# Optimization experiments

Measured on AMD Instinct MI355X. Metric: run time of the kernel, lower is better.

The kernel has to match this reference:

```python
import math
import jax, jax.numpy as jnp
import numpy as np

B, H, L, E = 2, 8, 2048, 64
MEM, LMEM = 512, 0
KV = L + MEM + LMEM


def rel_shift(x):
    # x: [..., i, j] -> Transformer-XL relative shift, output [..., i, j]
    *lead, i, j = x.shape
    x = jnp.concatenate([x, jnp.zeros((*lead, i, i), x.dtype)], axis=-1)  # [..., i, i+j]
    l = i + j - 1
    flat = x.reshape(*lead, i * (i + j))
    pad = (-flat.shape[-1]) % l
    flat = jnp.concatenate([flat, jnp.zeros((*lead, pad), x.dtype)], axis=-1)
    shifted = flat.reshape(*lead, -1, l)
    return shifted[..., :i, i - 1:]


def setup_inputs() -> dict:
    key = jax.random.key(0)
    kq, kk, kv, kp = jax.random.split(key, 4)
    return {
        "q": jax.random.normal(kq, (B, H, L, E), jnp.float32),
        "k": jax.random.normal(kk, (B, H, KV, E), jnp.float32),
        "v": jax.random.normal(kv, (B, H, KV, E), jnp.float32),
        "attn_mask": 0,
        "pos_emb": jax.random.normal(kp, (H, KV, E), jnp.float32),
        "kv_len": KV,
        "mem_len": MEM,
        "lmem_len": LMEM,
    }


def reference(q, k, v, attn_mask, pos_emb, kv_len, mem_len, lmem_len):
    b, h, l, e = q.shape
    scale = 1.0 / math.sqrt(e)
    dots = jnp.einsum('bhid,bhjd->bhij', q, k) * scale  # [B,H,L,KV]
    # relative-position bias
    pe = pos_emb[:, -kv_len:].astype(q.dtype)  # [H,KV,E]
    pos_dots = jnp.einsum('bhid,hjd->bhij', q, pe) * scale
    pos_dots = rel_shift(pos_dots)
    pad = dots.shape[-1] - pos_dots.shape[-1]
    pos_dots = jnp.pad(pos_dots, ((0, 0), (0, 0), (0, 0), (pad, 0)))
    dots = dots + pos_dots
    # memory-aware causal mask: [L, L+total_mem], triu at diag 1+total_mem
    total_mem = mem_len + lmem_len
    mask = jnp.triu(jnp.ones((l, l + total_mem), bool), k=1 + total_mem)
    neg = -jnp.finfo(dots.dtype).max
    dots = jnp.where(mask[None, None], neg, dots)
    attn = jax.nn.softmax(dots, axis=-1)  # dropout is identity at eval
    out = jnp.einsum('bhij,bhjd->bhid', attn, v)
    return out.transpose(0, 2, 1, 3).reshape(b, l, h * e)
```

## Files before the change

### kernel.cpp

```cpp
#include <hip/hip_runtime.h>
#include <hip/hip_bf16.h>

typedef __bf16 bf16;
typedef __attribute__((ext_vector_type(8))) __bf16 bf16x8;
typedef __attribute__((ext_vector_type(4))) __bf16 bf16x4;
typedef __attribute__((ext_vector_type(2))) __bf16 bf16x2;
typedef __attribute__((ext_vector_type(4))) float f32x4;

#define NB 2
#define NH 8
#define NL 2048
#define NE 64
#define NKV 2560

#define QN (NB*NH*NL*NE)
#define KN (NB*NH*NKV*NE)
#define VN KN
#define PEN (NH*NKV*NE)

#define MFMA(a,b,c) __builtin_amdgcn_mfma_f32_16x16x32_bf16(a,b,c,0,0,0)

template<int CTRL>
__device__ __forceinline__ float fdpp(float x) {
  return __builtin_bit_cast(float,
    __builtin_amdgcn_update_dpp(0, __builtin_bit_cast(int, x), CTRL, 0xF, 0xF, true));
}
__device__ __forceinline__ float rowmax16(float x) {
  x = fmaxf(x, fdpp<0x121>(x));
  x = fmaxf(x, fdpp<0x122>(x));
  x = fmaxf(x, fdpp<0x124>(x));
  x = fmaxf(x, fdpp<0x128>(x));
  return x;
}
__device__ __forceinline__ float rowsum16(float x) {
  x += fdpp<0x121>(x);
  x += fdpp<0x122>(x);
  x += fdpp<0x124>(x);
  x += fdpp<0x128>(x);
  return x;
}

extern "C" __global__ __launch_bounds__(256) void cvt_kernel(
    const float* __restrict__ q, const float* __restrict__ k,
    const float* __restrict__ v, const float* __restrict__ pe,
    bf16* __restrict__ ws)
{
  long i = ((long)blockIdx.x * 256 + threadIdx.x) * 8;
  const float* __restrict__ src;
  long off;
  if (i < QN)            { src = q;  off = i; }
  else if (i < QN+KN)    { src = k;  off = i - QN; }
  else if (i < QN+KN+VN) { src = v;  off = i - (QN+KN); }
  else                   { src = pe; off = i - (QN+KN+VN); }
  float4 f0 = *(const float4*)(src + off);
  float4 f1 = *(const float4*)(src + off + 4);
  bf16x8 o = { (bf16)f0.x, (bf16)f0.y, (bf16)f0.z, (bf16)f0.w,
               (bf16)f1.x, (bf16)f1.y, (bf16)f1.z, (bf16)f1.w };
  *(bf16x8*)(ws + i) = o;
}

extern "C" __global__ __launch_bounds__(256, 2) void attn_kernel(
    const bf16* __restrict__ qb, const bf16* __restrict__ kb,
    const bf16* __restrict__ vb, const bf16* __restrict__ peb,
    float* __restrict__ out)
{
  __shared__ bf16 Klds[64][72];
  __shared__ bf16 Vtlds[64][72];
  __shared__ bf16 PElds[128][72];
  __shared__ bf16 Plds[4][16][72];

  const int tid  = threadIdx.x;
  const int wave = tid >> 6;
  const int lane = tid & 63;
  const int g    = lane >> 4;
  const int c    = lane & 15;

  const int id   = blockIdx.x;
  const int jm   = id & 255;
  const int half = id >> 8;
  const int qtile = half ? (jm & 31) : (31 - (jm & 31));
  const int hb = (half << 3) | (jm >> 5);
  const int h  = hb & 7;
  const int b  = hb >> 3;
  const int bh = b * NH + h;
  const int r0  = qtile * 64;
  const int r0w = r0 + wave * 16;

  const bf16* __restrict__ qB  = qb  + (size_t)bh * NL  * NE;
  const bf16* __restrict__ kB  = kb  + (size_t)bh * NKV * NE;
  const bf16* __restrict__ vB  = vb  + (size_t)bh * NKV * NE;
  const bf16* __restrict__ peB = peb + (size_t)h  * NKV * NE;

  bf16x8 aq[2];
#pragma unroll
  for (int ks = 0; ks < 2; ++ks)
    aq[ks] = *(const bf16x8*)(qB + (size_t)(r0w + c) * NE + ks*32 + g*8);

  const f32x4 ZERO = {0.f, 0.f, 0.f, 0.f};
  f32x4 O[4];
  float M2[4], Lsum[4];
#pragma unroll
  for (int i = 0; i < 4; ++i) { O[i] = ZERO; M2[i] = -3.0e38f; Lsum[i] = 0.f; }

  const int ntiles = qtile + 9;
  const float COMB = 0.125f * 1.44269504088896f;

  bf16x8 sk0, sk1, svv0, svv1, spe0, spe1, spe2, spe3;
  const int krow = tid >> 2, kseg = tid & 3;
  const int vp   = tid >> 3, vcg  = tid & 7;
  const int perow = tid >> 1, peseg = tid & 1;

#define LOADT(m0_, pebase_) do {                                             \
    { const bf16* s = kB + (size_t)((m0_) + krow) * NE + kseg * 16;          \
      sk0 = *(const bf16x8*)(s); sk1 = *(const bf16x8*)(s + 8); }            \
    { const bf16* s = vB + (size_t)((m0_) + 2*vp) * NE + vcg * 8;            \
      svv0 = *(const bf16x8*)(s); svv1 = *(const bf16x8*)(s + NE); }         \
    { int prw = (pebase_) + perow;                                           \
      prw = prw < (NKV-1) ? prw : (NKV-1);                                   \
      const bf16* s = peB + (size_t)prw * NE + peseg * 32;                   \
      spe0 = *(const bf16x8*)(s);      spe1 = *(const bf16x8*)(s + 8);       \
      spe2 = *(const bf16x8*)(s + 16); spe3 = *(const bf16x8*)(s + 24); }    \
  } while (0)

  const int pebase0 = 1984 - r0;
  LOADT(0, pebase0);

  for (int t = 0; t < ntiles; ++t) {
    const int m0 = t * 64;

    __syncthreads();
    *(bf16x8*)&Klds[krow][kseg*16]   = sk0;
    *(bf16x8*)&Klds[krow][kseg*16+8] = sk1;
    {
      const int colw = (2*vp) ^ (vcg << 3);
#pragma unroll
      for (int i2 = 0; i2 < 8; ++i2) {
        bf16x2 pr = { svv0[i2], svv1[i2] };
        *(bf16x2*)&Vtlds[vcg*8 + i2][colw] = pr;
      }
    }
    *(bf16x8*)&PElds[perow][peseg*32]      = spe0;
    *(bf16x8*)&PElds[perow][peseg*32 + 8]  = spe1;
    *(bf16x8*)&PElds[perow][peseg*32 + 16] = spe2;
    *(bf16x8*)&PElds[perow][peseg*32 + 24] = spe3;
    __syncthreads();

    if (t + 1 < ntiles) LOADT(m0 + 64, pebase0 + m0 + 64);

    f32x4 S[4];
#pragma unroll
    for (int sub = 0; sub < 4; ++sub) {
      S[sub] = ZERO;
#pragma unroll
      for (int ks = 0; ks < 2; ++ks) {
        bf16x8 bk = *(const bf16x8*)&Klds[sub*16 + c][ks*32 + g*8];
        S[sub] = MFMA(aq[ks], bk, S[sub]);
      }
    }
    f32x4 PP[5];
    {
      const int bo = 48 - wave * 16;
#pragma unroll
      for (int sub = 0; sub < 5; ++sub) {
        PP[sub] = ZERO;
#pragma unroll
        for (int ks = 0; ks < 2; ++ks) {
          bf16x8 bp = *(const bf16x8*)&PElds[bo + sub*16 + c][ks*32 + g*8];
          PP[sub] = MFMA(aq[ks], bp, PP[sub]);
        }
      }
    }

    float sv[4][4];
#pragma unroll
    for (int reg = 0; reg < 4; ++reg) {
      const int qr = g*4 + reg;
      const int srcc = (c - qr + 15) & 15;
      float sh[5];
#pragma unroll
      for (int s5 = 0; s5 < 5; ++s5) sh[s5] = __shfl(PP[s5][reg], srcc, 16);
      const bool sel = (c > qr);
#pragma unroll
      for (int sub = 0; sub < 4; ++sub) {
        const float bias = sel ? sh[sub+1] : sh[sub];
        sv[sub][reg] = (S[sub][reg] + bias) * COMB;
      }
    }
    if (t == ntiles - 1) {
#pragma unroll
      for (int sub = 0; sub < 4; ++sub)
#pragma unroll
        for (int reg = 0; reg < 4; ++reg)
          if (sub*16 + c > wave*16 + g*4 + reg) sv[sub][reg] = -3.0e38f;
    }

    float pexp[4][4];
#pragma unroll
    for (int reg = 0; reg < 4; ++reg) {
      float m2 = fmaxf(fmaxf(sv[0][reg], sv[1][reg]), fmaxf(sv[2][reg], sv[3][reg]));
      m2 = rowmax16(m2);
      const float Mn = fmaxf(M2[reg], m2);
      const float alpha = exp2f(M2[reg] - Mn);
      float rs = 0.f;
#pragma unroll
      for (int sub = 0; sub < 4; ++sub) {
        float p = exp2f(sv[sub][reg] - Mn);
        pexp[sub][reg] = p;
        rs += p;
      }
      rs = rowsum16(rs);
      Lsum[reg] = Lsum[reg] * alpha + rs;
      M2[reg] = Mn;
#pragma unroll
      for (int es = 0; es < 4; ++es) O[es][reg] *= alpha;
    }

#pragma unroll
    for (int sub = 0; sub < 4; ++sub)
#pragma unroll
      for (int reg = 0; reg < 4; ++reg)
        Plds[wave][g*4 + reg][sub*16 + c] = (bf16)pexp[sub][reg];

    __builtin_amdgcn_wave_barrier();

#pragma unroll
    for (int ks = 0; ks < 2; ++ks) {
      bf16x8 ap = *(const bf16x8*)&Plds[wave][c][ks*32 + g*8];
#pragma unroll
      for (int es = 0; es < 4; ++es) {
        const int vrow = es*16 + c;
        const int vcol = (ks*32 + g*8) ^ ((vrow >> 3) << 3);
        bf16x8 bv = *(const bf16x8*)&Vtlds[vrow][vcol];
        O[es] = MFMA(ap, bv, O[es]);
      }
    }
  }

  float rinv[4];
#pragma unroll
  for (int reg = 0; reg < 4; ++reg) rinv[reg] = 1.0f / Lsum[reg];
#pragma unroll
  for (int es = 0; es < 4; ++es)
#pragma unroll
    for (int reg = 0; reg < 4; ++reg) {
      const int r = r0w + g*4 + reg;
      out[((size_t)b * NL + r) * (NH*NE) + h * NE + es*16 + c] = O[es][reg] * rinv[reg];
    }
}

extern "C" void kernel_launch(void* const* d_in, const int* in_sizes, int n_in,
                              void* d_out, int out_size, void* d_ws, size_t ws_size,
                              hipStream_t stream)
{
  const float* q  = (const float*)d_in[0];
  const float* k  = (const float*)d_in[1];
  const float* v  = (const float*)d_in[2];
  const float* pe = (const float*)d_in[4];
  float* out = (float*)d_out;
  bf16* ws = (bf16*)d_ws;

  cvt_kernel<<<4224, 256, 0, stream>>>(q, k, v, pe, ws);
  attn_kernel<<<512, 256, 0, stream>>>(
      ws, ws + QN, ws + QN + KN, ws + QN + KN + VN, out);
}
```

Before: 164.3 us.

## Pre-transpose V in convert kernel and double-buffer tiles via direct global-to-LDS loads

The convert kernel now writes V in a transposed [E][KV] layout through an LDS tile transpose, so the attention kernel no longer has to transpose V element-by-element into shared memory. The attention kernel stages K, V^T and positional-embedding tiles straight into double-buffered, XOR-swizzled LDS using global_load_lds, and overlaps the next tile's load with the current tile's compute using raw s_barrier and vmcnt waits. This removes the register round trip and the scattered bf16x2 LDS writes. In exchange it doubles LDS use, which may lower occupancy, and it relies on hand-written waitcnt counts being correct.

```diff
diff --git a/kernel.cpp b/kernel.cpp
--- a/kernel.cpp
+++ b/kernel.cpp
@@ -3,8 +3,6 @@
 
 typedef __bf16 bf16;
 typedef __attribute__((ext_vector_type(8))) __bf16 bf16x8;
-typedef __attribute__((ext_vector_type(4))) __bf16 bf16x4;
-typedef __attribute__((ext_vector_type(2))) __bf16 bf16x2;
 typedef __attribute__((ext_vector_type(4))) float f32x4;
 
 #define NB 2
@@ -19,6 +17,10 @@
 #define PEN (NH*NKV*NE)
 
 #define MFMA(a,b,c) __builtin_amdgcn_mfma_f32_16x16x32_bf16(a,b,c,0,0,0)
+
+#define GLOAD16(gp, lp) __builtin_amdgcn_global_load_lds(                   \
+    (const __attribute__((address_space(1))) void*)(gp),                    \
+    (__attribute__((address_space(3))) void*)(lp), 16, 0, 0)
 
 template<int CTRL>
 __device__ __forceinline__ float fdpp(float x) {
@@ -45,35 +47,68 @@
     const float* __restrict__ v, const float* __restrict__ pe,
     bf16* __restrict__ ws)
 {
-  long i = ((long)blockIdx.x * 256 + threadIdx.x) * 8;
-  const float* __restrict__ src;
-  long off;
-  if (i < QN)            { src = q;  off = i; }
-  else if (i < QN+KN)    { src = k;  off = i - QN; }
-  else if (i < QN+KN+VN) { src = v;  off = i - (QN+KN); }
-  else                   { src = pe; off = i - (QN+KN+VN); }
-  float4 f0 = *(const float4*)(src + off);
-  float4 f1 = *(const float4*)(src + off + 4);
-  bf16x8 o = { (bf16)f0.x, (bf16)f0.y, (bf16)f0.z, (bf16)f0.w,
-               (bf16)f1.x, (bf16)f1.y, (bf16)f1.z, (bf16)f1.w };
-  *(bf16x8*)(ws + i) = o;
+  __shared__ bf16 T[64][72];
+  const int bid = blockIdx.x, tid = threadIdx.x;
+  if (bid < 2944) {
+    long j = (long)bid * 2048 + tid * 8;
+    const float* __restrict__ src; bf16* __restrict__ dst;
+    if (j < QN)          { src = q + j;            dst = ws + j; }
+    else if (j < QN+KN)  { src = k + (j - QN);     dst = ws + j; }
+    else                 { src = pe + (j - QN - KN); dst = ws + j + VN; }
+    float4 f0 = *(const float4*)(src);
+    float4 f1 = *(const float4*)(src + 4);
+    bf16x8 o = { (bf16)f0.x, (bf16)f0.y, (bf16)f0.z, (bf16)f0.w,
+                 (bf16)f1.x, (bf16)f1.y, (bf16)f1.z, (bf16)f1.w };
+    *(bf16x8*)dst = o;
+  } else {
+    const int tb = bid - 2944;
+    const int bh = tb / 40, kt = tb % 40;
+    const float* __restrict__ vB = v + ((size_t)bh * NKV + kt * 64) * NE;
+    bf16* __restrict__ vT = ws + QN + KN + (size_t)bh * NE * NKV;
+    const int key = tid >> 2, e0 = (tid & 3) * 16;
+    const int sw = ((key >> 4) & 3) << 1;
+    const float* s = vB + (size_t)key * NE + e0;
+#pragma unroll
+    for (int j2 = 0; j2 < 2; ++j2) {
+      float4 fa = *(const float4*)(s + j2 * 8);
+      float4 fb = *(const float4*)(s + j2 * 8 + 4);
+      bf16x8 o = { (bf16)fa.x, (bf16)fa.y, (bf16)fa.z, (bf16)fa.w,
+                   (bf16)fb.x, (bf16)fb.y, (bf16)fb.z, (bf16)fb.w };
+      const int ch = (tid & 3) * 2 + j2;
+      *(bf16x8*)&T[key][(ch ^ sw) * 8] = o;
+    }
+    __syncthreads();
+    const int e = tid >> 2, ks0 = (tid & 3) * 16;
+#pragma unroll
+    for (int j2 = 0; j2 < 2; ++j2) {
+      bf16x8 o;
+#pragma unroll
+      for (int i = 0; i < 8; ++i) {
+        const int K = ks0 + j2 * 8 + i;
+        const int pos = (e >> 3) ^ (((K >> 4) & 3) << 1);
+        o[i] = T[K][pos * 8 + (e & 7)];
+      }
+      *(bf16x8*)&vT[(size_t)e * NKV + kt * 64 + ks0 + j2 * 8] = o;
+    }
+  }
 }
 
 extern "C" __global__ __launch_bounds__(256, 2) void attn_kernel(
     const bf16* __restrict__ qb, const bf16* __restrict__ kb,
-    const bf16* __restrict__ vb, const bf16* __restrict__ peb,
+    const bf16* __restrict__ vtb, const bf16* __restrict__ peb,
     float* __restrict__ out)
 {
-  __shared__ bf16 Klds[64][72];
-  __shared__ bf16 Vtlds[64][72];
-  __shared__ bf16 PElds[128][72];
-  __shared__ bf16 Plds[4][16][72];
+  __shared__ __align__(16) bf16 Kd[2][64][64];
+  __shared__ __align__(16) bf16 Vd[2][64][64];
+  __shared__ __align__(16) bf16 PEd[2][128][64];
+  __shared__ __align__(16) bf16 Plds[4][16][72];
 
   const int tid  = threadIdx.x;
   const int wave = tid >> 6;
   const int lane = tid & 63;
   const int g    = lane >> 4;
   const int c    = lane & 15;
+  const int cx   = c & 7;
 
   const int id   = blockIdx.x;
   const int jm   = id & 255;
@@ -88,7 +123,7 @@
 
   const bf16* __restrict__ qB  = qb  + (size_t)bh * NL  * NE;
   const bf16* __restrict__ kB  = kb  + (size_t)bh * NKV * NE;
-  const bf16* __restrict__ vB  = vb  + (size_t)bh * NKV * NE;
+  const bf16* __restrict__ vB  = vtb + (size_t)bh * NE  * NKV;
   const bf16* __restrict__ peB = peb + (size_t)h  * NKV * NE;
 
   bf16x8 aq[2];
@@ -104,48 +139,41 @@
 
   const int ntiles = qtile + 9;
   const float COMB = 0.125f * 1.44269504088896f;
-
-  bf16x8 sk0, sk1, svv0, svv1, spe0, spe1, spe2, spe3;
-  const int krow = tid >> 2, kseg = tid & 3;
-  const int vp   = tid >> 3, vcg  = tid & 7;
-  const int perow = tid >> 1, peseg = tid & 1;
-
-#define LOADT(m0_, pebase_) do {                                             \
-    { const bf16* s = kB + (size_t)((m0_) + krow) * NE + kseg * 16;          \
-      sk0 = *(const bf16x8*)(s); sk1 = *(const bf16x8*)(s + 8); }            \
-    { const bf16* s = vB + (size_t)((m0_) + 2*vp) * NE + vcg * 8;            \
-      svv0 = *(const bf16x8*)(s); svv1 = *(const bf16x8*)(s + NE); }         \
-    { int prw = (pebase_) + perow;                                           \
-      prw = prw < (NKV-1) ? prw : (NKV-1);                                   \
-      const bf16* s = peB + (size_t)prw * NE + peseg * 32;                   \
-      spe0 = *(const bf16x8*)(s);      spe1 = *(const bf16x8*)(s + 8);       \
-      spe2 = *(const bf16x8*)(s + 16); spe3 = *(const bf16x8*)(s + 24); }    \
+  const int pebase0 = 1984 - r0;
+
+  const int lr = lane >> 3;
+  const int lc = (lane & 7) ^ lr;
+
+#define STAGE(buf_, m0_, pebase_) do {                                         \
+    _Pragma("unroll")                                                          \
+    for (int j_ = 0; j_ < 2; ++j_) {                                           \
+      const int rb_ = (wave*2 + j_)*8;                                         \
+      GLOAD16(kB + (size_t)((m0_) + rb_ + lr)*NE + lc*8, &Kd[buf_][rb_][0]);   \
+      GLOAD16(vB + (size_t)(rb_ + lr)*NKV + (m0_) + lc*8, &Vd[buf_][rb_][0]);  \
+    }                                                                          \
+    _Pragma("unroll")                                                          \
+    for (int j_ = 0; j_ < 4; ++j_) {                                           \
+      const int rb_ = (wave*4 + j_)*8;                                         \
+      int prw_ = (pebase_) + rb_ + lr;                                         \
+      prw_ = prw_ < (NKV-1) ? prw_ : (NKV-1);                                  \
+      GLOAD16(peB + (size_t)prw_*NE + lc*8, &PEd[buf_][rb_][0]);               \
+    }                                                                          \
   } while (0)
 
-  const int pebase0 = 1984 - r0;
-  LOADT(0, pebase0);
+  STAGE(0, 0, pebase0);
 
   for (int t = 0; t < ntiles; ++t) {
-    const int m0 = t * 64;
-
-    __syncthreads();
-    *(bf16x8*)&Klds[krow][kseg*16]   = sk0;
-    *(bf16x8*)&Klds[krow][kseg*16+8] = sk1;
-    {
-      const int colw = (2*vp) ^ (vcg << 3);
-#pragma unroll
-      for (int i2 = 0; i2 < 8; ++i2) {
-        bf16x2 pr = { svv0[i2], svv1[i2] };
-        *(bf16x2*)&Vtlds[vcg*8 + i2][colw] = pr;
-      }
-    }
-    *(bf16x8*)&PElds[perow][peseg*32]      = spe0;
-    *(bf16x8*)&PElds[perow][peseg*32 + 8]  = spe1;
-    *(bf16x8*)&PElds[perow][peseg*32 + 16] = spe2;
-    *(bf16x8*)&PElds[perow][peseg*32 + 24] = spe3;
-    __syncthreads();
-
-    if (t + 1 < ntiles) LOADT(m0 + 64, pebase0 + m0 + 64);
+    const int cur = t & 1;
+    const int m0  = t * 64;
+
+    asm volatile("s_barrier" ::: "memory");
+    if (t + 1 < ntiles) {
+      STAGE(cur ^ 1, m0 + 64, pebase0 + m0 + 64);
+      asm volatile("s_waitcnt vmcnt(8)" ::: "memory");
+    } else {
+      asm volatile("s_waitcnt vmcnt(0)" ::: "memory");
+    }
+    asm volatile("s_barrier" ::: "memory");
 
     f32x4 S[4];
 #pragma unroll
@@ -153,7 +181,7 @@
       S[sub] = ZERO;
 #pragma unroll
       for (int ks = 0; ks < 2; ++ks) {
-        bf16x8 bk = *(const bf16x8*)&Klds[sub*16 + c][ks*32 + g*8];
+        bf16x8 bk = *(const bf16x8*)&Kd[cur][sub*16 + c][((ks*4 + g) ^ cx) * 8];
         S[sub] = MFMA(aq[ks], bk, S[sub]);
       }
     }
@@ -165,7 +193,7 @@
         PP[sub] = ZERO;
 #pragma unroll
         for (int ks = 0; ks < 2; ++ks) {
-          bf16x8 bp = *(const bf16x8*)&PElds[bo + sub*16 + c][ks*32 + g*8];
+          bf16x8 bp = *(const bf16x8*)&PEd[cur][bo + sub*16 + c][((ks*4 + g) ^ cx) * 8];
           PP[sub] = MFMA(aq[ks], bp, PP[sub]);
         }
       }
@@ -228,9 +256,7 @@
       bf16x8 ap = *(const bf16x8*)&Plds[wave][c][ks*32 + g*8];
 #pragma unroll
       for (int es = 0; es < 4; ++es) {
-        const int vrow = es*16 + c;
-        const int vcol = (ks*32 + g*8) ^ ((vrow >> 3) << 3);
-        bf16x8 bv = *(const bf16x8*)&Vtlds[vrow][vcol];
+        bf16x8 bv = *(const bf16x8*)&Vd[cur][es*16 + c][((ks*4 + g) ^ cx) * 8];
         O[es] = MFMA(ap, bv, O[es]);
       }
     }
@@ -259,7 +285,7 @@
   float* out = (float*)d_out;
   bf16* ws = (bf16*)d_ws;
 
-  cvt_kernel<<<4224, 256, 0, stream>>>(q, k, v, pe, ws);
+  cvt_kernel<<<3584, 256, 0, stream>>>(q, k, v, pe, ws);
   attn_kernel<<<512, 256, 0, stream>>>(
       ws, ws + QN, ws + QN + KN, ws + QN + KN + VN, out);
 }
```

Result: slower. 172.6 us (+5.1%).
